# Kernel tuning notes

Hardware: AMD Instinct MI355X
Metric: run time of the kernel (lower is better)

The kernel has to match this reference:

```python
import jax, jax.numpy as jnp
import numpy as np

N_EMBD = 1024
N_HEAD = 16
STRIDE = 128
C = 8
SEQ = 2048
BATCH = 2


def _sparse_causal_mask(nd, ns, stride, c, dtype):
    # Faithful vectorization of _sparse_attention_mask:
    # column j is globally visible if (j % stride) >= stride - c (the last c
    # columns of each stride block), each query also sees its own stride block,
    # and everything is causally masked (j <= q).
    j = jnp.arange(ns)
    q = jnp.arange(ns)[:, None]
    col_sel = (j % stride) >= (stride - c)          # strided summary columns
    same_block = (j[None, :] // stride) == (q // stride)  # local block
    causal = j[None, :] <= q
    mask = ((col_sel[None, :] | same_block) & causal).astype(dtype)
    return mask[ns - nd:]


def setup_inputs() -> dict:
    key = jax.random.key(0)
    k1, k2, k3 = jax.random.split(key, 3)
    inputs = jax.random.normal(k1, (BATCH, SEQ, N_EMBD), dtype=jnp.float32)
    w_attn = jax.random.normal(k2, (N_EMBD, 3 * N_EMBD), dtype=jnp.float32) * 0.02
    b_attn = jnp.zeros((3 * N_EMBD,), dtype=jnp.float32)
    proj_std = 0.02 / np.sqrt(2 * 24)  # n_layer = 24
    w_proj = jax.random.normal(k3, (N_EMBD, N_EMBD), dtype=jnp.float32) * proj_std
    b_proj = jnp.zeros((N_EMBD,), dtype=jnp.float32)
    return {"inputs": inputs, "w_attn": w_attn, "b_attn": b_attn,
            "w_proj": w_proj, "b_proj": b_proj}


def reference(inputs, w_attn, b_attn, w_proj, b_proj):
    B, S, E = inputs.shape
    H = N_HEAD
    D = E // H
    qkv = inputs @ w_attn + b_attn                     # [B,S,3E]
    q, k, v = jnp.split(qkv, 3, axis=-1)
    def split_heads(x):
        return x.reshape(B, S, H, D).transpose(0, 2, 1, 3)  # [B,H,S,D]
    q, k, v = split_heads(q), split_heads(k), split_heads(v)
    present = jnp.stack([k, v], axis=1)                # [B,2,H,S,D]
    scale = jnp.asarray(D, q.dtype) ** 0.5
    w = jnp.einsum('bhqd,bhkd->bhqk', q, k) / scale    # [B,H,S,S]
    mask = _sparse_causal_mask(S, S, STRIDE, C, w.dtype)
    w = w * mask - 1e10 * (1.0 - mask)
    p = jax.nn.softmax(w, axis=-1).astype(v.dtype)
    h = jnp.einsum('bhqk,bhkd->bhqd', p, v)            # [B,H,S,D]
    h = h.transpose(0, 2, 1, 3).reshape(B, S, E)       # merge heads
    h = h @ w_proj + b_proj
    # dropout p=0.0 (eval) -> identity
    return (h, present)
```

## Files before the change

kernel.cpp:

```cpp
#include <hip/hip_runtime.h>
#include <stdint.h>

typedef unsigned short u16;
typedef unsigned int u32;
typedef __attribute__((ext_vector_type(4))) float f32x4;
typedef __attribute__((ext_vector_type(4))) u16 u16x4;
typedef __attribute__((ext_vector_type(8))) __bf16 bf16x8;

__device__ __forceinline__ u16 f2bf(float f) {
  u32 u = __builtin_bit_cast(u32, f);
  u = (u + 0x7FFFu + ((u >> 16) & 1u)) >> 16;
  return (u16)u;
}

__device__ __forceinline__ void gload_lds16(const void* g, void* l) {
  __builtin_amdgcn_global_load_lds(
      (const __attribute__((address_space(1))) void*)(uintptr_t)(g),
      (__attribute__((address_space(3))) void*)(u32)(uintptr_t)(l),
      16, 0, 0);
}

__global__ __launch_bounds__(256) void k_prep(
    const float* __restrict__ x, u16* __restrict__ xbf,
    const float* __restrict__ wa, u16* __restrict__ wat,
    const float* __restrict__ wp, u16* __restrict__ wpt) {
  __shared__ float tile[32][33];
  const int bid = blockIdx.x, t = threadIdx.x;
  if (bid < 4096) {
    int i = bid * 256 + t;
    f32x4 v = ((const f32x4*)x)[i];
    u16x4 o = { f2bf(v.x), f2bf(v.y), f2bf(v.z), f2bf(v.w) };
    ((u16x4*)xbf)[i] = o;
    return;
  }
  const float* in;
  u16* out;
  int n0, k0, N;
  if (bid < 4096 + 3072) {
    int idx = bid - 4096;
    in = wa; out = wat; N = 3072;
    n0 = (idx % 96) * 32; k0 = (idx / 96) * 32;
  } else {
    int idx = bid - 7168;
    in = wp; out = wpt; N = 1024;
    n0 = (idx & 31) * 32; k0 = (idx >> 5) * 32;
  }
  int c = t & 31, r0 = t >> 5;
#pragma unroll
  for (int i = 0; i < 4; ++i)
    tile[r0 + i * 8][c] = in[(size_t)(k0 + r0 + i * 8) * N + n0 + c];
  __syncthreads();
  int on = t >> 3, ok = (t & 7) * 4;
  u16x4 o = { f2bf(tile[ok + 0][on]), f2bf(tile[ok + 1][on]),
              f2bf(tile[ok + 2][on]), f2bf(tile[ok + 3][on]) };
  *(u16x4*)&out[(size_t)(n0 + on) * 1024 + k0 + ok] = o;
}

__global__ __launch_bounds__(256) void k_kv(const float* __restrict__ present,
                                            u16* __restrict__ kbf,
                                            u16* __restrict__ vtw) {
  __shared__ float tile[32][33];
  const int bid = blockIdx.x, t = threadIdx.x;
  if (bid >= 4096) {
    int i = bid - 4096;
    size_t idx = (size_t)i * 256 + t;
    size_t b = idx >> 19, off = idx & ((1u << 19) - 1);
    f32x4 v = ((const f32x4*)present)[b * (1u << 20) + off];
    u16x4 o = { f2bf(v.x), f2bf(v.y), f2bf(v.z), f2bf(v.w) };
    ((u16x4*)kbf)[idx] = o;
    return;
  }
  int bh = bid >> 7, rem = bid & 127;
  int s0 = (rem >> 1) * 32, d0 = (rem & 1) * 32;
  int b = bh >> 4, h = bh & 15;
  const float* vsrc = present + (((size_t)(b * 2 + 1) * 16 + h) * 2048) * 64;
  u16* vdst = vtw + ((size_t)bh * 64) * 2048;
  int c = t & 31, r0 = t >> 5;
#pragma unroll
  for (int i = 0; i < 4; ++i)
    tile[r0 + i * 8][c] = vsrc[(size_t)(s0 + r0 + i * 8) * 64 + d0 + c];
  __syncthreads();
  int on = t >> 3, ok = (t & 7) * 4;
  u16x4 o = { f2bf(tile[ok + 0][on]), f2bf(tile[ok + 1][on]),
              f2bf(tile[ok + 2][on]), f2bf(tile[ok + 3][on]) };
  *(u16x4*)&vdst[(size_t)(d0 + on) * 2048 + s0 + ok] = o;
}

__global__ __launch_bounds__(512, 1) void k_gemm256(
    const u16* __restrict__ A, const u16* __restrict__ Bt,
    const float* __restrict__ bias, u16* __restrict__ outq,
    float* __restrict__ outp) {
  __shared__ u16 a_lds[2][256 * 64];
  __shared__ u16 b_lds[2][192 * 64];
  const int t = threadIdx.x;
  const int lane = t & 63, w = t >> 6;
  const int cc = lane & 15, g = lane >> 4;
  const int wr = w >> 2, wc = w & 3;

  int f = blockIdx.y * 16 + blockIdx.x;
  int xcd = f & 7, idx = f >> 3;
  const int m0 = ((xcd >> 1) * 4 + (idx >> 3)) * 256;
  const int n0 = ((xcd & 1) * 8 + (idx & 7)) * 192;

  const int srow = t >> 3;
  const int scolb = (t & 7) * 16;
  const size_t pitch = 2048;

  auto stageB = [&](int bi, int kt) {
#pragma unroll
    for (int i = 0; i < 3; ++i) {
      int row = i * 64 + srow;
      gload_lds16((const char*)Bt + (size_t)(n0 + row) * pitch + kt * 128 +
                      (scolb ^ ((row & 7) << 4)),
                  (char*)b_lds[bi] + row * 128 + scolb);
    }
  };
  auto stageA2 = [&](int bi, int kt, int half) {
#pragma unroll
    for (int i = 0; i < 2; ++i) {
      int row = (half * 2 + i) * 64 + srow;
      gload_lds16((const char*)A + (size_t)(m0 + row) * pitch + kt * 128 +
                      (scolb ^ ((row & 7) << 4)),
                  (char*)a_lds[bi] + row * 128 + scolb);
    }
  };

  f32x4 acc[8][3] = {};

  stageB(0, 0);
  stageA2(0, 0, 0);
  stageA2(0, 0, 1);
  asm volatile("s_waitcnt vmcnt(0)\n\ts_barrier" ::: "memory");

  for (int j = 0; j < 16; ++j) {
    const int bi = j & 1, nx = bi ^ 1;

    bf16x8 bfr[3][2];
#pragma unroll
    for (int q = 0; q < 4; ++q) {
      if (j < 15) {
        if (q == 0) stageB(nx, j + 1);
        else if (q == 1) stageA2(nx, j + 1, 0);
        else if (q == 2) stageA2(nx, j + 1, 1);
      }
      if (q == 0) {
#pragma unroll
        for (int nf = 0; nf < 3; ++nf) {
          int row = wc * 48 + nf * 16 + cc;
#pragma unroll
          for (int kk = 0; kk < 2; ++kk)
            bfr[nf][kk] =
                *(const bf16x8*)((const char*)b_lds[bi] + row * 128 +
                                 ((kk * 64 + g * 16) ^ ((row & 7) << 4)));
        }
      }
      bf16x8 af[2][2];
#pragma unroll
      for (int mf = 0; mf < 2; ++mf) {
        int row = wr * 128 + q * 32 + mf * 16 + cc;
#pragma unroll
        for (int kk = 0; kk < 2; ++kk)
          af[mf][kk] = *(const bf16x8*)((const char*)a_lds[bi] + row * 128 +
                                        ((kk * 64 + g * 16) ^ ((row & 7) << 4)));
      }
      __builtin_amdgcn_s_setprio(1);
#pragma unroll
      for (int mf = 0; mf < 2; ++mf)
#pragma unroll
        for (int nf = 0; nf < 3; ++nf)
#pragma unroll
          for (int kk = 0; kk < 2; ++kk)
            acc[q * 2 + mf][nf] = __builtin_amdgcn_mfma_f32_16x16x32_bf16(
                af[mf][kk], bfr[nf][kk], acc[q * 2 + mf][nf], 0, 0, 0);
      __builtin_amdgcn_s_setprio(0);
      if (q < 3) {
        __builtin_amdgcn_s_barrier();
      } else if (j < 15) {
        asm volatile("s_waitcnt vmcnt(0)\n\ts_barrier" ::: "memory");
      }
    }
  }

  float bv[3];
#pragma unroll
  for (int nf = 0; nf < 3; ++nf) bv[nf] = bias[n0 + wc * 48 + nf * 16 + cc];

#pragma unroll
  for (int mf = 0; mf < 8; ++mf)
#pragma unroll
    for (int nf = 0; nf < 3; ++nf) {
      int n = n0 + wc * 48 + nf * 16 + cc;
      int mb = m0 + wr * 128 + mf * 16 + g * 4;
      float v[4];
#pragma unroll
      for (int j = 0; j < 4; ++j) v[j] = acc[mf][nf][j] + bv[nf];
      if (n < 1024) {
#pragma unroll
        for (int j = 0; j < 4; ++j) outq[(size_t)(mb + j) * 1024 + n] = f2bf(v[j]);
      } else {
        int n2 = n - 1024;
        int kv = n2 >> 10; n2 &= 1023;
        int hh = n2 >> 6, d = n2 & 63;
        int bb = mb >> 11, ss = mb & 2047;
        float* pr = outp + ((((size_t)bb * 2 + kv) * 16 + hh) * 2048 + ss) * 64 + d;
#pragma unroll
        for (int j = 0; j < 4; ++j) pr[(size_t)j * 64] = v[j];
      }
    }
}

template <int EPI, int BN>
__global__ __launch_bounds__(256) void k_gemm(
    const u16* __restrict__ A, const u16* __restrict__ Bt,
    const float* __restrict__ bias, u16* __restrict__ outq,
    float* __restrict__ outp, int M, int N, int K) {
  __shared__ u16 a_lds[128 * 64];
  __shared__ u16 b_lds[BN * 64];
  const int t = threadIdx.x;
  const int lane = t & 63, w = t >> 6;

  int m0, n0;
  {
    constexpr int NXT = (EPI == 0) ? 24 : 16;
    constexpr int NCH = (EPI == 0) ? 12 : 8;
    int f = blockIdx.y * NXT + blockIdx.x;
    int xcd = f & 7, idx = f >> 3;
    int mt = (xcd >> 1) * 8 + idx / NCH;
    int nt = (xcd & 1) * NCH + idx % NCH;
    m0 = mt * 128;
    n0 = nt * BN;
  }

  const int srow = t >> 3;
  const int scb = (t & 7) * 16;
  const int ssw = scb ^ ((srow & 7) << 4);
  const size_t pitch = (size_t)K * 2;
  const char* aS = (const char*)A + (size_t)(m0 + srow) * pitch + ssw;
  const char* bS = (const char*)Bt + (size_t)(n0 + srow) * pitch + ssw;
  char* al = (char*)a_lds + t * 16;
  char* bl = (char*)b_lds + t * 16;
  const int wm = (w >> 1) * 64, wn = (w & 1) * (BN / 2);
  const int cc = lane & 15, g = lane >> 4;
  constexpr int NF = BN / 32;

  f32x4 acc[4][NF] = {};

  for (int kt = 0; kt < K; kt += 64) {
    __syncthreads();
#pragma unroll
    for (int i = 0; i < 4; ++i)
      gload_lds16(aS + (size_t)kt * 2 + (size_t)i * 32 * pitch, al + i * 4096);
#pragma unroll
    for (int i = 0; i < BN / 32; ++i)
      gload_lds16(bS + (size_t)kt * 2 + (size_t)i * 32 * pitch, bl + i * 4096);
    __syncthreads();
#pragma unroll
    for (int kk = 0; kk < 2; ++kk) {
      bf16x8 af[4], bf_[NF];
#pragma unroll
      for (int mf = 0; mf < 4; ++mf) {
        int row = wm + mf * 16 + cc;
        af[mf] = *(const bf16x8*)((const char*)a_lds + row * 128 +
                                  ((kk * 64 + g * 16) ^ ((row & 7) << 4)));
      }
#pragma unroll
      for (int nf = 0; nf < NF; ++nf) {
        int row = wn + nf * 16 + cc;
        bf_[nf] = *(const bf16x8*)((const char*)b_lds + row * 128 +
                                   ((kk * 64 + g * 16) ^ ((row & 7) << 4)));
      }
#pragma unroll
      for (int mf = 0; mf < 4; ++mf)
#pragma unroll
        for (int nf = 0; nf < NF; ++nf)
          acc[mf][nf] = __builtin_amdgcn_mfma_f32_16x16x32_bf16(
              af[mf], bf_[nf], acc[mf][nf], 0, 0, 0);
    }
  }

  float bv[NF];
#pragma unroll
  for (int nf = 0; nf < NF; ++nf) bv[nf] = bias[n0 + wn + nf * 16 + cc];

#pragma unroll
  for (int mf = 0; mf < 4; ++mf)
#pragma unroll
    for (int nf = 0; nf < NF; ++nf) {
      int n = n0 + wn + nf * 16 + cc;
      int mb = m0 + wm + mf * 16 + g * 4;
      float v[4];
#pragma unroll
      for (int j = 0; j < 4; ++j) v[j] = acc[mf][nf][j] + bv[nf];
      if (EPI == 1) {
#pragma unroll
        for (int j = 0; j < 4; ++j) outp[(size_t)(mb + j) * N + n] = v[j];
      } else if (n < 1024) {
#pragma unroll
        for (int j = 0; j < 4; ++j) outq[(size_t)(mb + j) * 1024 + n] = f2bf(v[j]);
      } else {
        int n2 = n - 1024;
        int kv = n2 >> 10; n2 &= 1023;
        int hh = n2 >> 6, d = n2 & 63;
        int bb = mb >> 11, ss = mb & 2047;
        float* pr = outp + ((((size_t)bb * 2 + kv) * 16 + hh) * 2048 + ss) * 64 + d;
#pragma unroll
        for (int j = 0; j < 4; ++j) pr[(size_t)j * 64] = v[j];
      }
    }
}

__global__ __launch_bounds__(256) void k_attn(
    const u16* __restrict__ qws, const u16* __restrict__ kbf,
    const u16* __restrict__ vtw, u16* __restrict__ hws) {
  const int qb = blockIdx.x, h = blockIdx.y, b = blockIdx.z;
  const int t = threadIdx.x, lane = t & 63, w = t >> 6;
  const int cc = lane & 15, g = lane >> 4;

  __shared__ u16 k_lds[256 * 64];
  __shared__ u16 p_lds[4][32 * 72];
  __shared__ float rsum[4][32];

  const char* kh = (const char*)kbf + (size_t)(b * 16 + h) * (2048 * 128);
  const char* vh = (const char*)vtw + (size_t)(b * 16 + h) * (64 * 4096);

  {
    int rr = t >> 3, seg = (t & 7) * 16;
#pragma unroll
    for (int i = 0; i < 8; ++i) {
      int r = i * 32 + rr;
      int i2 = r - 128;
      int gr = (r < 128) ? (qb * 128 + r) : ((i2 >> 3) * 128 + 120 + (i2 & 7));
      gload_lds16(kh + (size_t)gr * 128 + (seg ^ ((r & 7) << 4)),
                  (char*)k_lds + i * 4096 + t * 16);
    }
  }

  bf16x8 qf_[2][2];
  {
    const char* qsrc = (const char*)qws +
        (size_t)(b * 2048 + qb * 128 + w * 32 + cc) * 2048 + h * 128 + g * 16;
#pragma unroll
    for (int qf = 0; qf < 2; ++qf)
#pragma unroll
      for (int kk = 0; kk < 2; ++kk)
        qf_[qf][kk] = *(const bf16x8*)(qsrc + (size_t)qf * 16 * 2048 + kk * 64);
  }
  __syncthreads();

  const int nsum = 8 * qb;
  f32x4 o_[2][4] = {};
  float lsum[2] = { 0.f, 0.f };

#pragma unroll 2
  for (int ch = 0; ch < 4; ++ch) {
    f32x4 s[4][2] = {};
#pragma unroll
    for (int kf2 = 0; kf2 < 4; ++kf2) {
      int row = ch * 64 + kf2 * 16 + cc;
      const char* kr = (const char*)k_lds + row * 128;
#pragma unroll
      for (int kk = 0; kk < 2; ++kk) {
        bf16x8 kfr = *(const bf16x8*)(kr + ((kk * 64 + g * 16) ^ ((cc & 7) << 4)));
#pragma unroll
        for (int qf = 0; qf < 2; ++qf)
          s[kf2][qf] = __builtin_amdgcn_mfma_f32_16x16x32_bf16(
              kfr, qf_[qf][kk], s[kf2][qf], 0, 0, 0);
      }
    }
#pragma unroll
    for (int qf = 0; qf < 2; ++qf) {
      int q_local = w * 32 + qf * 16 + cc;
#pragma unroll
      for (int kf2 = 0; kf2 < 4; ++kf2) {
#pragma unroll
        for (int j = 0; j < 4; ++j) {
          int key = ch * 64 + kf2 * 16 + g * 4 + j;
          bool vis = (key < 128) ? (key <= q_local) : (key - 128 < nsum);
          float p = vis ? exp2f(s[kf2][qf][j] * 0.180336884f) : 0.f;
          s[kf2][qf][j] = p;
          lsum[qf] += p;
        }
        u16x4 pw = { f2bf(s[kf2][qf][0]), f2bf(s[kf2][qf][1]),
                     f2bf(s[kf2][qf][2]), f2bf(s[kf2][qf][3]) };
        *(u16x4*)&p_lds[w][(qf * 16 + cc) * 72 + kf2 * 16 + g * 4] = pw;
      }
    }
#pragma unroll
    for (int kk = 0; kk < 2; ++kk) {
      bf16x8 pa[2], vb[4];
#pragma unroll
      for (int mf = 0; mf < 2; ++mf)
        pa[mf] = *(const bf16x8*)((const char*)p_lds[w] +
                                  (mf * 16 + cc) * 144 + kk * 64 + g * 16);
      int cb = (ch < 2) ? (qb * 256 + ch * 128 + kk * 64 + g * 16)
                        : (((ch - 2) * 8 + kk * 4 + g) * 256 + 240);
#pragma unroll
      for (int nf = 0; nf < 4; ++nf)
        vb[nf] = *(const bf16x8*)(vh + (size_t)(nf * 16 + cc) * 4096 + cb);
#pragma unroll
      for (int mf = 0; mf < 2; ++mf)
#pragma unroll
        for (int nf = 0; nf < 4; ++nf)
          o_[mf][nf] = __builtin_amdgcn_mfma_f32_16x16x32_bf16(pa[mf], vb[nf],
                                                               o_[mf][nf], 0, 0, 0);
    }
  }

#pragma unroll
  for (int qf = 0; qf < 2; ++qf) {
    float sum = lsum[qf];
    sum += __shfl_xor(sum, 16);
    sum += __shfl_xor(sum, 32);
    if (g == 0) rsum[w][qf * 16 + cc] = sum;
  }
#pragma unroll
  for (int mf = 0; mf < 2; ++mf)
#pragma unroll
    for (int j = 0; j < 4; ++j) {
      float inv = 1.0f / rsum[w][mf * 16 + g * 4 + j];
      size_t row = (size_t)(b * 2048 + qb * 128 + w * 32 + mf * 16 + g * 4 + j);
#pragma unroll
      for (int nf = 0; nf < 4; ++nf)
        hws[row * 1024 + h * 64 + nf * 16 + cc] = f2bf(o_[mf][nf][j] * inv);
    }
}

extern "C" void kernel_launch(void* const* d_in, const int* in_sizes, int n_in,
                              void* d_out, int out_size, void* d_ws, size_t ws_size,
                              hipStream_t stream) {
  const float* x      = (const float*)d_in[0];
  const float* w_attn = (const float*)d_in[1];
  const float* b_attn = (const float*)d_in[2];
  const float* w_proj = (const float*)d_in[3];
  const float* b_proj = (const float*)d_in[4];
  float* h_out   = (float*)d_out;
  float* present = (float*)d_out + 4194304;

  char* ws = (char*)d_ws;
  u16* xbf = (u16*)(ws);
  u16* qws = (u16*)(ws + (8u << 20));
  u16* wat = (u16*)(ws + (16u << 20));
  u16* wpt = (u16*)(ws + (22u << 20));
  u16* kbf = (u16*)(ws + (24u << 20));
  u16* vtw = (u16*)(ws + (32u << 20));
  u16* hws = xbf;

  k_prep<<<8192, 256, 0, stream>>>(x, xbf, w_attn, wat, w_proj, wpt);
  k_gemm256<<<dim3(16, 16), 512, 0, stream>>>(xbf, wat, b_attn, qws, present);
  k_kv<<<8192, 256, 0, stream>>>(present, kbf, vtw);
  k_attn<<<dim3(16, 16, 2), 256, 0, stream>>>(qws, kbf, vtw, hws);
  k_gemm<1, 64><<<dim3(16, 32), 256, 0, stream>>>(hws, wpt, b_proj, nullptr,
                                                  h_out, 4096, 1024, 1024);
}
```

Measured before the change: 87.02 us.

## Restructure QKV GEMM warp tiling to 4x2 and software-pipeline LDS fragment reads

Changes the per-warp tile of the 256x192 QKV GEMM from 128x48 (2x4 warp grid) to 64x96 (4x2 warp grid). The main loop now issues all global-to-LDS staging at once per K-step, with one barrier instead of four. LDS fragment loads for the second K-half and the next tile are prefetched into registers so they overlap with MFMA work. The aim is fewer barriers and better overlap of LDS reads with matrix math. The cost is more live registers for the double-buffered fragments.

```diff
diff --git a/kernel.cpp b/kernel.cpp
--- a/kernel.cpp
+++ b/kernel.cpp
@@ -95,7 +95,7 @@
   const int t = threadIdx.x;
   const int lane = t & 63, w = t >> 6;
   const int cc = lane & 15, g = lane >> 4;
-  const int wr = w >> 2, wc = w & 3;
+  const int wr = w >> 1, wc = w & 1;
 
   int f = blockIdx.y * 16 + blockIdx.x;
   int xcd = f & 7, idx = f >> 3;
@@ -106,7 +106,7 @@
   const int scolb = (t & 7) * 16;
   const size_t pitch = 2048;
 
-  auto stageB = [&](int bi, int kt) {
+  auto stage = [&](int bi, int kt) {
 #pragma unroll
     for (int i = 0; i < 3; ++i) {
       int row = i * 64 + srow;
@@ -114,83 +114,81 @@
                       (scolb ^ ((row & 7) << 4)),
                   (char*)b_lds[bi] + row * 128 + scolb);
     }
-  };
-  auto stageA2 = [&](int bi, int kt, int half) {
-#pragma unroll
-    for (int i = 0; i < 2; ++i) {
-      int row = (half * 2 + i) * 64 + srow;
+#pragma unroll
+    for (int i = 0; i < 4; ++i) {
+      int row = i * 64 + srow;
       gload_lds16((const char*)A + (size_t)(m0 + row) * pitch + kt * 128 +
                       (scolb ^ ((row & 7) << 4)),
                   (char*)a_lds[bi] + row * 128 + scolb);
     }
   };
 
-  f32x4 acc[8][3] = {};
-
-  stageB(0, 0);
-  stageA2(0, 0, 0);
-  stageA2(0, 0, 1);
+  auto readA = [&](bf16x8 (&af)[4], int bi, int kk) {
+#pragma unroll
+    for (int mf = 0; mf < 4; ++mf) {
+      int row = wr * 64 + mf * 16 + cc;
+      af[mf] = *(const bf16x8*)((const char*)a_lds[bi] + row * 128 +
+                                ((kk * 64 + g * 16) ^ ((row & 7) << 4)));
+    }
+  };
+  auto readB = [&](bf16x8 (&bf)[6], int bi, int kk) {
+#pragma unroll
+    for (int nf = 0; nf < 6; ++nf) {
+      int row = wc * 96 + nf * 16 + cc;
+      bf[nf] = *(const bf16x8*)((const char*)b_lds[bi] + row * 128 +
+                                ((kk * 64 + g * 16) ^ ((row & 7) << 4)));
+    }
+  };
+
+  f32x4 acc[4][6] = {};
+  bf16x8 a0[4], b0[6], a1[4], b1[6];
+
+  stage(0, 0);
   asm volatile("s_waitcnt vmcnt(0)\n\ts_barrier" ::: "memory");
+  readA(a0, 0, 0);
+  readB(b0, 0, 0);
 
   for (int j = 0; j < 16; ++j) {
     const int bi = j & 1, nx = bi ^ 1;
-
-    bf16x8 bfr[3][2];
-#pragma unroll
-    for (int q = 0; q < 4; ++q) {
-      if (j < 15) {
-        if (q == 0) stageB(nx, j + 1);
-        else if (q == 1) stageA2(nx, j + 1, 0);
-        else if (q == 2) stageA2(nx, j + 1, 1);
-      }
-      if (q == 0) {
-#pragma unroll
-        for (int nf = 0; nf < 3; ++nf) {
-          int row = wc * 48 + nf * 16 + cc;
-#pragma unroll
-          for (int kk = 0; kk < 2; ++kk)
-            bfr[nf][kk] =
-                *(const bf16x8*)((const char*)b_lds[bi] + row * 128 +
-                                 ((kk * 64 + g * 16) ^ ((row & 7) << 4)));
-        }
-      }
-      bf16x8 af[2][2];
-#pragma unroll
-      for (int mf = 0; mf < 2; ++mf) {
-        int row = wr * 128 + q * 32 + mf * 16 + cc;
-#pragma unroll
-        for (int kk = 0; kk < 2; ++kk)
-          af[mf][kk] = *(const bf16x8*)((const char*)a_lds[bi] + row * 128 +
-                                        ((kk * 64 + g * 16) ^ ((row & 7) << 4)));
-      }
-      __builtin_amdgcn_s_setprio(1);
-#pragma unroll
-      for (int mf = 0; mf < 2; ++mf)
-#pragma unroll
-        for (int nf = 0; nf < 3; ++nf)
-#pragma unroll
-          for (int kk = 0; kk < 2; ++kk)
-            acc[q * 2 + mf][nf] = __builtin_amdgcn_mfma_f32_16x16x32_bf16(
-                af[mf][kk], bfr[nf][kk], acc[q * 2 + mf][nf], 0, 0, 0);
-      __builtin_amdgcn_s_setprio(0);
-      if (q < 3) {
-        __builtin_amdgcn_s_barrier();
-      } else if (j < 15) {
-        asm volatile("s_waitcnt vmcnt(0)\n\ts_barrier" ::: "memory");
-      }
-    }
-  }
-
-  float bv[3];
-#pragma unroll
-  for (int nf = 0; nf < 3; ++nf) bv[nf] = bias[n0 + wc * 48 + nf * 16 + cc];
-
-#pragma unroll
-  for (int mf = 0; mf < 8; ++mf)
-#pragma unroll
-    for (int nf = 0; nf < 3; ++nf) {
-      int n = n0 + wc * 48 + nf * 16 + cc;
-      int mb = m0 + wr * 128 + mf * 16 + g * 4;
+    if (j < 15) stage(nx, j + 1);
+    readA(a1, bi, 1);
+    readB(b1, bi, 1);
+
+    __builtin_amdgcn_s_setprio(1);
+#pragma unroll
+    for (int mf = 0; mf < 4; ++mf)
+#pragma unroll
+      for (int nf = 0; nf < 6; ++nf)
+        acc[mf][nf] = __builtin_amdgcn_mfma_f32_16x16x32_bf16(
+            a0[mf], b0[nf], acc[mf][nf], 0, 0, 0);
+    __builtin_amdgcn_s_setprio(0);
+
+    __builtin_amdgcn_s_setprio(1);
+#pragma unroll
+    for (int mf = 0; mf < 4; ++mf)
+#pragma unroll
+      for (int nf = 0; nf < 6; ++nf)
+        acc[mf][nf] = __builtin_amdgcn_mfma_f32_16x16x32_bf16(
+            a1[mf], b1[nf], acc[mf][nf], 0, 0, 0);
+    __builtin_amdgcn_s_setprio(0);
+
+    if (j < 15) {
+      asm volatile("s_waitcnt vmcnt(0) lgkmcnt(0)\n\ts_barrier" ::: "memory");
+      readA(a0, nx, 0);
+      readB(b0, nx, 0);
+    }
+  }
+
+  float bv[6];
+#pragma unroll
+  for (int nf = 0; nf < 6; ++nf) bv[nf] = bias[n0 + wc * 96 + nf * 16 + cc];
+
+#pragma unroll
+  for (int mf = 0; mf < 4; ++mf)
+#pragma unroll
+    for (int nf = 0; nf < 6; ++nf) {
+      int n = n0 + wc * 96 + nf * 16 + cc;
+      int mb = m0 + wr * 64 + mf * 16 + g * 4;
       float v[4];
 #pragma unroll
       for (int j = 0; j < 4; ++j) v[j] = acc[mf][nf][j] + bv[nf];
```

Result: no change. 86.50 us (median of 3 runs) (-0.6%).

## Reorder A-tile row ownership and use partial vmcnt waits in QKV GEMM

Applied to the files above, without the earlier changes.

Changes how rows of the A tile map to waves in the 256x192 QKV GEMM, so that each quarter step q reads a contiguous 64-row band that lines up with the two-half A staging. The full `vmcnt(0)` drain at the end of each k-step is replaced with partial waits (`vmcnt(5)` at q==1, `vmcnt(2)` at q==3). This lets the second half of the next A tile stay in flight while the first half is already being consumed. An extra barrier with an LDS wait and a sched_barrier is added before each MFMA batch. The intent is to hide global-to-LDS load latency, at the cost of one more barrier per quarter step and correctness that depends on exact load counts.

```diff
diff --git a/kernel.cpp b/kernel.cpp
--- a/kernel.cpp
+++ b/kernel.cpp
@@ -95,7 +95,7 @@
   const int t = threadIdx.x;
   const int lane = t & 63, w = t >> 6;
   const int cc = lane & 15, g = lane >> 4;
-  const int wr = w >> 2, wc = w & 3;
+  const int wr2 = w >> 2, wc = w & 3;
 
   int f = blockIdx.y * 16 + blockIdx.x;
   int xcd = f & 7, idx = f >> 3;
@@ -115,10 +115,10 @@
                   (char*)b_lds[bi] + row * 128 + scolb);
     }
   };
-  auto stageA2 = [&](int bi, int kt, int half) {
+  auto stageA = [&](int bi, int kt, int half) {
 #pragma unroll
     for (int i = 0; i < 2; ++i) {
-      int row = (half * 2 + i) * 64 + srow;
+      int row = half * 128 + i * 64 + srow;
       gload_lds16((const char*)A + (size_t)(m0 + row) * pitch + kt * 128 +
                       (scolb ^ ((row & 7) << 4)),
                   (char*)a_lds[bi] + row * 128 + scolb);
@@ -126,22 +126,21 @@
   };
 
   f32x4 acc[8][3] = {};
+  bf16x8 bfr[3][2];
 
   stageB(0, 0);
-  stageA2(0, 0, 0);
-  stageA2(0, 0, 1);
+  stageA(0, 0, 0);
+  stageA(0, 0, 1);
   asm volatile("s_waitcnt vmcnt(0)\n\ts_barrier" ::: "memory");
 
-  for (int j = 0; j < 16; ++j) {
-    const int bi = j & 1, nx = bi ^ 1;
-
-    bf16x8 bfr[3][2];
+  for (int kt = 0; kt < 16; ++kt) {
+    const int bi = kt & 1, nx = bi ^ 1;
 #pragma unroll
     for (int q = 0; q < 4; ++q) {
-      if (j < 15) {
-        if (q == 0) stageB(nx, j + 1);
-        else if (q == 1) stageA2(nx, j + 1, 0);
-        else if (q == 2) stageA2(nx, j + 1, 1);
+      if (kt < 15) {
+        if (q == 0) stageB(nx, kt + 1);
+        else if (q == 1) stageA(nx, kt + 1, 0);
+        else if (q == 2) stageA(nx, kt + 1, 1);
       }
       if (q == 0) {
 #pragma unroll
@@ -157,12 +156,15 @@
       bf16x8 af[2][2];
 #pragma unroll
       for (int mf = 0; mf < 2; ++mf) {
-        int row = wr * 128 + q * 32 + mf * 16 + cc;
+        int row = q * 64 + wr2 * 32 + mf * 16 + cc;
 #pragma unroll
         for (int kk = 0; kk < 2; ++kk)
           af[mf][kk] = *(const bf16x8*)((const char*)a_lds[bi] + row * 128 +
                                         ((kk * 64 + g * 16) ^ ((row & 7) << 4)));
       }
+      asm volatile("s_barrier" ::: "memory");
+      asm volatile("s_waitcnt lgkmcnt(0)" ::: "memory");
+      __builtin_amdgcn_sched_barrier(0);
       __builtin_amdgcn_s_setprio(1);
 #pragma unroll
       for (int mf = 0; mf < 2; ++mf)
@@ -173,11 +175,12 @@
             acc[q * 2 + mf][nf] = __builtin_amdgcn_mfma_f32_16x16x32_bf16(
                 af[mf][kk], bfr[nf][kk], acc[q * 2 + mf][nf], 0, 0, 0);
       __builtin_amdgcn_s_setprio(0);
-      if (q < 3) {
-        __builtin_amdgcn_s_barrier();
-      } else if (j < 15) {
-        asm volatile("s_waitcnt vmcnt(0)\n\ts_barrier" ::: "memory");
-      }
+      if (q == 1)
+        asm volatile("s_waitcnt vmcnt(5)\n\ts_barrier" ::: "memory");
+      else if (q == 3)
+        asm volatile("s_waitcnt vmcnt(2)\n\ts_barrier" ::: "memory");
+      else
+        asm volatile("s_barrier" ::: "memory");
     }
   }
 
@@ -186,14 +189,14 @@
   for (int nf = 0; nf < 3; ++nf) bv[nf] = bias[n0 + wc * 48 + nf * 16 + cc];
 
 #pragma unroll
-  for (int mf = 0; mf < 8; ++mf)
+  for (int a = 0; a < 8; ++a)
 #pragma unroll
     for (int nf = 0; nf < 3; ++nf) {
       int n = n0 + wc * 48 + nf * 16 + cc;
-      int mb = m0 + wr * 128 + mf * 16 + g * 4;
+      int mb = m0 + (a >> 1) * 64 + wr2 * 32 + (a & 1) * 16 + g * 4;
       float v[4];
 #pragma unroll
-      for (int j = 0; j < 4; ++j) v[j] = acc[mf][nf][j] + bv[nf];
+      for (int j = 0; j < 4; ++j) v[j] = acc[a][nf][j] + bv[nf];
       if (n < 1024) {
 #pragma unroll
         for (int j = 0; j < 4; ++j) outq[(size_t)(mb + j) * 1024 + n] = f2bf(v[j]);
```

Measured after the change: 88.26 us. Within noise of the previous version (+1.4%).
